# Kernel optimization log

Measured on AMD Instinct MI355X. Metric: run time of the kernel, lower is better.

The kernel has to match this reference:

```python
import jax, jax.numpy as jnp
import numpy as np

NUM_HEADS = 16

def setup_inputs() -> dict:
    key = jax.random.key(0)
    k1, k2, k3 = jax.random.split(key, 3)
    B, N, D = 2, 2048, 1024
    x = jax.random.normal(k1, (B, N, D), dtype=jnp.float32)
    w_qkv = jax.random.normal(k2, (D, 3 * D), dtype=jnp.float32) * (D ** -0.5)
    w_out = jax.random.normal(k3, (D, D), dtype=jnp.float32) * (D ** -0.5)
    return {"x": x, "w_qkv": w_qkv, "w_out": w_out}

def reference(x, w_qkv, w_out):
    B, N, D = x.shape
    H = NUM_HEADS
    d = D // H
    scale = d ** -0.5
    qkv = x @ w_qkv  # [B, N, 3D]
    q, k, v = jnp.split(qkv, 3, axis=-1)
    # b n (h d) -> b h n d
    split_heads = lambda t: t.reshape(B, N, H, d).transpose(0, 2, 1, 3)
    q, k, v = split_heads(q), split_heads(k), split_heads(v)
    dots = jnp.einsum('bhid,bhjd->bhij', q, k) * scale
    # causal mask: -inf above the diagonal
    causal = jnp.tril(jnp.ones((N, N), dtype=bool))
    dots = jnp.where(causal, dots, jnp.float32(-jnp.inf))
    attn = jax.nn.softmax(dots, axis=-1)
    out = jnp.einsum('bhij,bhjd->bhid', attn, v)
    out = out.transpose(0, 2, 1, 3).reshape(B, N, D)  # b h n d -> b n (h d)
    return out @ w_out
```

## Files before the change

### kernel.cpp

```cpp
#include <hip/hip_runtime.h>


typedef __bf16 bf16x8 __attribute__((ext_vector_type(8)));
typedef float f32x4 __attribute__((ext_vector_type(4)));
typedef unsigned int uint4v __attribute__((ext_vector_type(4)));

#define MFMA16(a, b, c) __builtin_amdgcn_mfma_f32_16x16x32_bf16((a), (b), (c), 0, 0, 0)

#define LDS_FENCE()                                   \
  do {                                                \
    asm volatile("s_waitcnt lgkmcnt(0)" ::: "memory");\
    __builtin_amdgcn_sched_barrier(0);                \
  } while (0)

__device__ __forceinline__ unsigned short f2bf(float f) {
  __bf16 h = (__bf16)f;
  return *(unsigned short*)&h;
}

__device__ __forceinline__ bf16x8 ones_frag() {
  uint4v u = {0x3F803F80u, 0x3F803F80u, 0x3F803F80u, 0x3F803F80u};
  return __builtin_bit_cast(bf16x8, u);
}

__global__ __launch_bounds__(256) void prep_kernel(
    const float* __restrict__ x, const float* __restrict__ wqkv,
    const float* __restrict__ wout, unsigned short* __restrict__ xb,
    unsigned short* __restrict__ wqkvT, unsigned short* __restrict__ woutT) {
  __shared__ float tile[32][33];
  const int id = blockIdx.x, t = threadIdx.x;
  if (id < 4096) {
    const int i = id * 256 + t;
    float4 v = ((const float4*)x)[i];
    ushort4 o;
    o.x = f2bf(v.x); o.y = f2bf(v.y); o.z = f2bf(v.z); o.w = f2bf(v.w);
    ((ushort4*)xb)[i] = o;
    return;
  }
  const int tx = t & 31, ty = t >> 5;
  const float* in; unsigned short* out;
  int C, scale_rows, bx, by;
  if (id < 7168) {
    const int q = id - 4096;
    in = wqkv; out = wqkvT; C = 3072; scale_rows = 1024;
    bx = q % 96; by = q / 96;
  } else {
    const int q = id - 7168;
    in = wout; out = woutT; C = 1024; scale_rows = 0;
    bx = q & 31; by = q >> 5;
  }
#pragma unroll
  for (int i = ty; i < 32; i += 8)
    tile[i][tx] = in[(size_t)(by * 32 + i) * C + bx * 32 + tx];
  __syncthreads();
#pragma unroll
  for (int i = ty; i < 32; i += 8) {
    const int orow = bx * 32 + i;
    const float s = (orow < scale_rows) ? 0.18033688f : 1.0f;
    out[(size_t)orow * 1024 + by * 32 + tx] = f2bf(tile[tx][i] * s);
  }
}

template <int MODE>
__global__ __launch_bounds__(256) void gemm128_kernel(
    const unsigned short* __restrict__ A,
    const unsigned short* __restrict__ BT,
    void* __restrict__ Cp, unsigned short* __restrict__ vTp,
    int M, int Nc, int K, int NX) {
  const int id0 = blockIdx.x;
  const int swz = (id0 & 7) * ((int)gridDim.x >> 3) + (id0 >> 3);
  const int bx = swz % NX, by = swz / NX;

  __shared__ unsigned short lA[128 * 64];
  __shared__ unsigned short lB[128 * 64];
  const int t = threadIdx.x;
  const int l = t & 63, g = l >> 4, c = l & 15;
  const int w = t >> 6;
  const int wm = (w >> 1) * 64, wn = (w & 1) * 64;
  const int bm = by * 128, bn = bx * 128;
  const int c7s = (c & 7);

  f32x4 acc[4][4] = {};

  for (int kk = 0; kk < K; kk += 64) {
    __syncthreads();
#pragma unroll
    for (int rd = 0; rd < 4; ++rd) {
      const int idx = rd * 256 + t;
      const int row = idx >> 3, ch = idx & 7;
      const int sc = (ch ^ (row & 7)) * 8;
      __builtin_amdgcn_global_load_lds(
          (const __attribute__((address_space(1))) void*)(
              A + (size_t)(bm + row) * K + kk + sc),
          (__attribute__((address_space(3))) void*)(lA + (idx & ~63) * 8),
          16, 0, 0);
      __builtin_amdgcn_global_load_lds(
          (const __attribute__((address_space(1))) void*)(
              BT + (size_t)(bn + row) * K + kk + sc),
          (__attribute__((address_space(3))) void*)(lB + (idx & ~63) * 8),
          16, 0, 0);
    }
    __syncthreads();

#pragma unroll
    for (int hh = 0; hh < 2; ++hh) {
      bf16x8 af[4], bfr[4];
#pragma unroll
      for (int mi = 0; mi < 4; ++mi)
        af[mi] = *(const bf16x8*)(lA + (wm + mi * 16 + c) * 64 +
                                  (((hh * 4 + g) ^ c7s) * 8));
#pragma unroll
      for (int ni = 0; ni < 4; ++ni)
        bfr[ni] = *(const bf16x8*)(lB + (wn + ni * 16 + c) * 64 +
                                   (((hh * 4 + g) ^ c7s) * 8));
#pragma unroll
      for (int mi = 0; mi < 4; ++mi)
#pragma unroll
        for (int ni = 0; ni < 4; ++ni)
          acc[mi][ni] = MFMA16(af[mi], bfr[ni], acc[mi][ni]);
    }
  }

  if (MODE == 0) {
    float* Cf = (float*)Cp;
#pragma unroll
    for (int mi = 0; mi < 4; ++mi)
#pragma unroll
      for (int r = 0; r < 4; ++r) {
        const int gr = bm + wm + mi * 16 + g * 4 + r;
#pragma unroll
        for (int ni = 0; ni < 4; ++ni)
          Cf[(size_t)gr * Nc + bn + wn + ni * 16 + c] = acc[mi][ni][r];
      }
  } else if (MODE == 2 && bn >= 2048) {
    const int bq = bm >> 11;
    const int nbase = bm - bq * 2048 + wm;
#pragma unroll
    for (int mi = 0; mi < 4; ++mi)
#pragma unroll
      for (int ni = 0; ni < 4; ++ni) {
        const int dimg = bn - 2048 + wn + ni * 16 + c;
        ushort4 pk;
        pk.x = f2bf(acc[mi][ni][0]); pk.y = f2bf(acc[mi][ni][1]);
        pk.z = f2bf(acc[mi][ni][2]); pk.w = f2bf(acc[mi][ni][3]);
        *(ushort4*)(vTp + ((size_t)(bq * 1024 + dimg)) * 2048 + nbase +
                    mi * 16 + g * 4) = pk;
      }
  } else {
    unsigned short* Cc = (unsigned short*)Cp;
#pragma unroll
    for (int mi = 0; mi < 4; ++mi)
#pragma unroll
      for (int r = 0; r < 4; ++r) {
        const int gr = bm + wm + mi * 16 + g * 4 + r;
#pragma unroll
        for (int ni = 0; ni < 4; ++ni)
          Cc[(size_t)gr * Nc + bn + wn + ni * 16 + c] = f2bf(acc[mi][ni][r]);
      }
  }
}

__global__ __launch_bounds__(256) void attn_kernel(
    const unsigned short* __restrict__ qkv,
    const unsigned short* __restrict__ vT,
    unsigned short* __restrict__ aout) {
  const int t = threadIdx.x, w = t >> 6, l = t & 63, g = l >> 4, c = l & 15;
  const int g4 = g * 4, c7 = c & 7;

  const int id0 = blockIdx.x;
  const int xcd = id0 & 7, pos = id0 >> 3;
  const int bh = xcd * 4 + (pos & 3);
  const int tile = 31 - (pos >> 2);
  const int b = bh >> 4, h = bh & 15;

  __shared__ __align__(16) unsigned short lK[2][64][64];
  __shared__ __align__(16) unsigned short lV[2][64][64];
  __shared__ __align__(16) unsigned short pl[4][16][72];

  const unsigned short* Qbase = qkv + (size_t)b * 2048 * 3072 + h * 64;
  const unsigned short* Kb = Qbase + 1024;
  const unsigned short* Vb = vT + ((size_t)b * 1024 + h * 64) * 2048;
  const bf16x8 vones = ones_frag();

#define KFRAG(row, half) (*(const bf16x8*)(Kb + (size_t)(row) * 3072 + (half) * 32 + g * 8))
#define VFRAG(dt, kvoff) (*(const bf16x8*)(Vb + (size_t)((dt) * 16 + c) * 2048 + (kvoff) + g * 8))

#define STAGE(dK, dV, kb_)                                                    \
  do {                                                                        \
    _Pragma("unroll")                                                         \
    for (int q = 0; q < 2; ++q) {                                             \
      const int idx = q * 256 + t;                                            \
      const int row = idx >> 3, ch = idx & 7;                                 \
      const int sc = (ch ^ (row & 7)) * 8;                                    \
      __builtin_amdgcn_global_load_lds(                                       \
          (const __attribute__((address_space(1))) void*)(                    \
              Kb + (size_t)(kb_ + row) * 3072 + sc),                          \
          (__attribute__((address_space(3))) void*)(                          \
              &(dK)[0][0] + (idx & ~63) * 8), 16, 0, 0);                      \
      __builtin_amdgcn_global_load_lds(                                       \
          (const __attribute__((address_space(1))) void*)(                    \
              Vb + (size_t)row * 2048 + (kb_) + sc),                          \
          (__attribute__((address_space(3))) void*)(                          \
              &(dV)[0][0] + (idx & ~63) * 8), 16, 0, 0);                      \
    }                                                                         \
  } while (0)

  const int q0 = tile * 64 + w * 16;
  const int qc = q0 + c;

  const bf16x8 bq0 = *(const bf16x8*)(Qbase + (size_t)qc * 3072 + g * 8);
  const bf16x8 bq1 = *(const bf16x8*)(Qbase + (size_t)qc * 3072 + 32 + g * 8);

  f32x4 o[4] = {};
  f32x4 dsum = {};

  if (tile > 0) {
    STAGE(lK[0], lV[0], 0);
    int cur = 0;
#pragma unroll 1
    for (int jb = 0; jb < tile; ++jb) {
      __syncthreads();
      if (jb + 1 < tile) STAGE(lK[cur ^ 1], lV[cur ^ 1], (jb + 1) * 64);

      const unsigned short* lk = &lK[cur][0][0];
      const unsigned short* lv = &lV[cur][0][0];

      bf16x8 ka[8];
#pragma unroll
      for (int n = 0; n < 4; ++n) {
        ka[2 * n]     = *(const bf16x8*)(lk + (16 * n + c) * 64 + ((g ^ c7) * 8));
        ka[2 * n + 1] = *(const bf16x8*)(lk + (16 * n + c) * 64 + (((4 + g) ^ c7) * 8));
      }
      bf16x8 bv[2][4];
#pragma unroll
      for (int ks = 0; ks < 2; ++ks)
#pragma unroll
        for (int dt = 0; dt < 4; ++dt)
          bv[ks][dt] = *(const bf16x8*)(lv + (dt * 16 + c) * 64 + (((ks * 4 + g) ^ c7) * 8));

      f32x4 s[4] = {};
#pragma unroll
      for (int n = 0; n < 4; ++n) {
        s[n] = MFMA16(ka[2 * n], bq0, s[n]);
        s[n] = MFMA16(ka[2 * n + 1], bq1, s[n]);
      }

#pragma unroll
      for (int n = 0; n < 4; ++n)
#pragma unroll
        for (int r = 0; r < 4; ++r)
          s[n][r] = exp2f(s[n][r]);

      LDS_FENCE();
#pragma unroll
      for (int n = 0; n < 4; ++n) {
        ushort4 pw;
        pw.x = f2bf(s[n][0]); pw.y = f2bf(s[n][1]);
        pw.z = f2bf(s[n][2]); pw.w = f2bf(s[n][3]);
        *(ushort4*)&pl[w][c][n * 16 + g4] = pw;
      }
      LDS_FENCE();
      const bf16x8 pa0 = *(const bf16x8*)&pl[w][c][g * 8];
      const bf16x8 pa1 = *(const bf16x8*)&pl[w][c][32 + g * 8];

      dsum = MFMA16(pa0, vones, dsum);
      dsum = MFMA16(pa1, vones, dsum);
#pragma unroll
      for (int dt = 0; dt < 4; ++dt) {
        o[dt] = MFMA16(pa0, bv[0][dt], o[dt]);
        o[dt] = MFMA16(pa1, bv[1][dt], o[dt]);
      }
      cur ^= 1;
    }
  }

  const int ndiag = 1 + (w >> 1);
#pragma unroll 1
  for (int j = 0; j < ndiag; ++j) {
    const int kb = tile * 64 + j * 32;
    const bf16x8 k00 = KFRAG(kb + c, 0), k01 = KFRAG(kb + c, 1);
    const bf16x8 k10 = KFRAG(kb + 16 + c, 0), k11 = KFRAG(kb + 16 + c, 1);
    const bf16x8 bv0 = VFRAG(0, kb), bv1 = VFRAG(1, kb);
    const bf16x8 bv2 = VFRAG(2, kb), bv3 = VFRAG(3, kb);

    f32x4 s0 = {}, s1 = {};
    s0 = MFMA16(k00, bq0, s0);
    s0 = MFMA16(k01, bq1, s0);
    s1 = MFMA16(k10, bq0, s1);
    s1 = MFMA16(k11, bq1, s1);

    float p0[4], p1[4];
#pragma unroll
    for (int r = 0; r < 4; ++r) {
      p0[r] = (kb + g4 + r <= qc) ? exp2f(s0[r]) : 0.0f;
      p1[r] = (kb + 16 + g4 + r <= qc) ? exp2f(s1[r]) : 0.0f;
    }

    LDS_FENCE();
    ushort4 pw;
    pw.x = f2bf(p0[0]); pw.y = f2bf(p0[1]); pw.z = f2bf(p0[2]); pw.w = f2bf(p0[3]);
    *(ushort4*)&pl[w][c][g4] = pw;
    pw.x = f2bf(p1[0]); pw.y = f2bf(p1[1]); pw.z = f2bf(p1[2]); pw.w = f2bf(p1[3]);
    *(ushort4*)&pl[w][c][16 + g4] = pw;
    LDS_FENCE();
    const bf16x8 pa = *(const bf16x8*)&pl[w][c][g * 8];

    dsum = MFMA16(pa, vones, dsum);
    o[0] = MFMA16(pa, bv0, o[0]);
    o[1] = MFMA16(pa, bv1, o[1]);
    o[2] = MFMA16(pa, bv2, o[2]);
    o[3] = MFMA16(pa, bv3, o[3]);
  }

#pragma unroll
  for (int r = 0; r < 4; ++r) {
    const float invr = 1.0f / dsum[r];
    const size_t row = (size_t)(b * 2048 + q0 + g4 + r);
#pragma unroll
    for (int dt = 0; dt < 4; ++dt)
      aout[row * 1024 + h * 64 + dt * 16 + c] = f2bf(o[dt][r] * invr);
  }
#undef KFRAG
#undef VFRAG
#undef STAGE
}

extern "C" void kernel_launch(void* const* d_in, const int* in_sizes, int n_in,
                              void* d_out, int out_size, void* d_ws, size_t ws_size,
                              hipStream_t stream) {
  const float* x = (const float*)d_in[0];
  const float* wqkv = (const float*)d_in[1];
  const float* wout = (const float*)d_in[2];
  float* out = (float*)d_out;

  unsigned short* ws = (unsigned short*)d_ws;
  unsigned short* xb = ws;
  unsigned short* wqkvT = xb + (size_t)4096 * 1024;
  unsigned short* woutT = wqkvT + (size_t)3072 * 1024;
  unsigned short* qkv = woutT + (size_t)1024 * 1024;
  unsigned short* vT = qkv + (size_t)4096 * 3072;
  unsigned short* aout = vT + (size_t)2 * 1024 * 2048;

  prep_kernel<<<8192, 256, 0, stream>>>(x, wqkv, wout, xb, wqkvT, woutT);
  gemm128_kernel<2><<<768, 256, 0, stream>>>(xb, wqkvT, qkv, vT, 4096, 3072, 1024, 24);
  attn_kernel<<<1024, 256, 0, stream>>>(qkv, vT, aout);
  gemm128_kernel<0><<<256, 256, 0, stream>>>(aout, woutT, out, nullptr, 4096, 1024, 1024, 8);
}
```

Before: 108.5 us.

## Replace QKV GEMM with 256x256 tile, 8-wave, double-buffered direct-to-LDS pipeline

The QKV projection GEMM moves from a 128x128, 4-wave kernel to a dedicated 256x256, 8-wave kernel. Tiles are loaded with global_load_lds straight into swizzled, double-buffered LDS, and the MFMA quadrants are interleaved with the next tile's loads, using barriers and s_setprio to overlap memory and compute. The goal is more operand reuse per LDS byte and hidden global load latency. In exchange the grid shrinks to 192 blocks, which fills fewer CUs on a 256-CU part, and register pressure at 512 threads is high.

```diff
diff --git a/kernel.cpp b/kernel.cpp
--- a/kernel.cpp
+++ b/kernel.cpp
@@ -61,12 +61,175 @@
   }
 }
 
-template <int MODE>
+__global__ __launch_bounds__(512) void gemm256_kernel(
+    const unsigned short* __restrict__ A,
+    const unsigned short* __restrict__ BT,
+    unsigned short* __restrict__ Cc,
+    unsigned short* __restrict__ vTp) {
+  const int id0 = blockIdx.x;
+  const int swz = (id0 & 7) * 24 + (id0 >> 3);
+  const int bx = swz % 12, by = swz / 12;
+  const int bm = by * 256, bn = bx * 256;
+
+  __shared__ unsigned short sA[2][2][128 * 64];
+  __shared__ unsigned short sB[2][2][128 * 64];
+
+  const int t = threadIdx.x;
+  const int l = t & 63, g = l >> 4, c = l & 15, c7 = c & 7;
+  const int wid = t >> 6, wr = wid >> 2, wc = wid & 3;
+
+  f32x4 acc[8][4] = {};
+  bf16x8 af[4][2], bfr[4][2];
+
+#define STG(dst, Mat, rowb, kt)                                               \
+  do {                                                                        \
+    _Pragma("unroll")                                                         \
+    for (int qq = 0; qq < 2; ++qq) {                                          \
+      const int idx = qq * 512 + t;                                           \
+      const int row = idx >> 3;                                               \
+      const int sc = ((idx & 7) ^ (row & 7)) * 8;                             \
+      __builtin_amdgcn_global_load_lds(                                       \
+          (const __attribute__((address_space(1))) void*)(                    \
+              (Mat) + (size_t)((rowb) + row) * 1024 + (kt) * 64 + sc),        \
+          (__attribute__((address_space(3))) void*)((dst) + (idx & ~63) * 8), \
+          16, 0, 0);                                                          \
+    }                                                                         \
+  } while (0)
+
+#define LDAQ(buf, qd)                                                         \
+  do {                                                                        \
+    _Pragma("unroll")                                                         \
+    for (int mi = 0; mi < 4; ++mi) {                                          \
+      const unsigned short* p =                                               \
+          &sA[buf][wr][0] + ((qd) * 64 + mi * 16 + c) * 64;                   \
+      af[mi][0] = *(const bf16x8*)(p + (g ^ c7) * 8);                         \
+      af[mi][1] = *(const bf16x8*)(p + ((4 + g) ^ c7) * 8);                   \
+    }                                                                         \
+  } while (0)
+
+#define LDBQ(buf, qd)                                                         \
+  do {                                                                        \
+    _Pragma("unroll")                                                         \
+    for (int nj = 0; nj < 2; ++nj) {                                          \
+      const unsigned short* p =                                               \
+          &sB[buf][wc >> 1][0] +                                              \
+          ((wc & 1) * 64 + ((qd) * 2 + nj) * 16 + c) * 64;                    \
+      bfr[(qd) * 2 + nj][0] = *(const bf16x8*)(p + (g ^ c7) * 8);             \
+      bfr[(qd) * 2 + nj][1] = *(const bf16x8*)(p + ((4 + g) ^ c7) * 8);       \
+    }                                                                         \
+  } while (0)
+
+#define MFMAQ(qm, qn)                                                         \
+  do {                                                                        \
+    _Pragma("unroll")                                                         \
+    for (int mi = 0; mi < 4; ++mi) {                                          \
+      _Pragma("unroll")                                                       \
+      for (int nj = 0; nj < 2; ++nj) {                                        \
+        f32x4 a0 = acc[(qm) * 4 + mi][(qn) * 2 + nj];                         \
+        a0 = MFMA16(af[mi][0], bfr[(qn) * 2 + nj][0], a0);                    \
+        a0 = MFMA16(af[mi][1], bfr[(qn) * 2 + nj][1], a0);                    \
+        acc[(qm) * 4 + mi][(qn) * 2 + nj] = a0;                               \
+      }                                                                       \
+    }                                                                         \
+  } while (0)
+
+#define BAR_OPEN()                                          \
+  do {                                                      \
+    __builtin_amdgcn_sched_barrier(0);                      \
+    __builtin_amdgcn_s_barrier();                           \
+    asm volatile("s_waitcnt lgkmcnt(0)" ::: "memory");      \
+    __builtin_amdgcn_sched_barrier(0);                      \
+    __builtin_amdgcn_s_setprio(1);                          \
+  } while (0)
+
+#define BAR_CLOSE()                                         \
+  do {                                                      \
+    __builtin_amdgcn_s_setprio(0);                          \
+    __builtin_amdgcn_sched_barrier(0);                      \
+    __builtin_amdgcn_s_barrier();                           \
+  } while (0)
+
+#define VMW4() asm volatile("s_waitcnt vmcnt(4)" ::: "memory")
+
+  STG(&sB[0][0][0], BT, bn, 0);
+  STG(&sB[0][1][0], BT, bn + 128, 0);
+  STG(&sA[0][0][0], A, bm, 0);
+  STG(&sA[0][1][0], A, bm + 128, 0);
+  STG(&sB[1][0][0], BT, bn, 1);
+  STG(&sB[1][1][0], BT, bn + 128, 1);
+  VMW4();
+  __builtin_amdgcn_s_barrier();
+
+#pragma unroll 1
+  for (int it = 0; it < 8; ++it) {
+    const int kt1 = 2 * it + 1;
+    const int kt2 = (2 * it + 2 < 15) ? 2 * it + 2 : 15;
+    const int kt3 = (2 * it + 3 < 15) ? 2 * it + 3 : 15;
+    LDAQ(0, 0); LDBQ(0, 0);
+    STG(&sA[1][0][0], A, bm, kt1);
+    BAR_OPEN(); MFMAQ(0, 0); BAR_CLOSE();
+    LDBQ(0, 1);
+    STG(&sA[1][1][0], A, bm + 128, kt1);
+    BAR_OPEN(); MFMAQ(0, 1); BAR_CLOSE();
+    LDAQ(0, 1);
+    STG(&sB[0][0][0], BT, bn, kt2);
+    BAR_OPEN(); MFMAQ(1, 0); BAR_CLOSE();
+    STG(&sB[0][1][0], BT, bn + 128, kt2);
+    VMW4();
+    BAR_OPEN(); MFMAQ(1, 1); BAR_CLOSE();
+    LDAQ(1, 0); LDBQ(1, 0);
+    STG(&sA[0][0][0], A, bm, kt2);
+    BAR_OPEN(); MFMAQ(0, 0); BAR_CLOSE();
+    LDBQ(1, 1);
+    STG(&sA[0][1][0], A, bm + 128, kt2);
+    BAR_OPEN(); MFMAQ(0, 1); BAR_CLOSE();
+    LDAQ(1, 1);
+    STG(&sB[1][0][0], BT, bn, kt3);
+    BAR_OPEN(); MFMAQ(1, 0); BAR_CLOSE();
+    STG(&sB[1][1][0], BT, bn + 128, kt3);
+    VMW4();
+    BAR_OPEN(); MFMAQ(1, 1); BAR_CLOSE();
+  }
+
+  if (bn >= 2048) {
+    const int bq = bm >> 11;
+    const int nb = (bm & 2047) + wr * 128;
+#pragma unroll
+    for (int mi8 = 0; mi8 < 8; ++mi8)
+#pragma unroll
+      for (int ni = 0; ni < 4; ++ni) {
+        const int dimg = bn - 2048 + wc * 64 + ni * 16 + c;
+        ushort4 pk;
+        pk.x = f2bf(acc[mi8][ni][0]); pk.y = f2bf(acc[mi8][ni][1]);
+        pk.z = f2bf(acc[mi8][ni][2]); pk.w = f2bf(acc[mi8][ni][3]);
+        *(ushort4*)(vTp + ((size_t)(bq * 1024 + dimg)) * 2048 + nb +
+                    mi8 * 16 + g * 4) = pk;
+      }
+  } else {
+#pragma unroll
+    for (int mi8 = 0; mi8 < 8; ++mi8)
+#pragma unroll
+      for (int r = 0; r < 4; ++r) {
+        const int gr = bm + wr * 128 + mi8 * 16 + g * 4 + r;
+#pragma unroll
+        for (int ni = 0; ni < 4; ++ni)
+          Cc[(size_t)gr * 3072 + bn + wc * 64 + ni * 16 + c] =
+              f2bf(acc[mi8][ni][r]);
+      }
+  }
+#undef STG
+#undef LDAQ
+#undef LDBQ
+#undef MFMAQ
+#undef BAR_OPEN
+#undef BAR_CLOSE
+#undef VMW4
+}
+
 __global__ __launch_bounds__(256) void gemm128_kernel(
     const unsigned short* __restrict__ A,
     const unsigned short* __restrict__ BT,
-    void* __restrict__ Cp, unsigned short* __restrict__ vTp,
-    int M, int Nc, int K, int NX) {
+    float* __restrict__ Cf, int M, int Nc, int K, int NX) {
   const int id0 = blockIdx.x;
   const int swz = (id0 & 7) * ((int)gridDim.x >> 3) + (id0 >> 3);
   const int bx = swz % NX, by = swz / NX;
@@ -121,43 +284,15 @@
     }
   }
 
-  if (MODE == 0) {
-    float* Cf = (float*)Cp;
-#pragma unroll
-    for (int mi = 0; mi < 4; ++mi)
-#pragma unroll
-      for (int r = 0; r < 4; ++r) {
-        const int gr = bm + wm + mi * 16 + g * 4 + r;
-#pragma unroll
-        for (int ni = 0; ni < 4; ++ni)
-          Cf[(size_t)gr * Nc + bn + wn + ni * 16 + c] = acc[mi][ni][r];
-      }
-  } else if (MODE == 2 && bn >= 2048) {
-    const int bq = bm >> 11;
-    const int nbase = bm - bq * 2048 + wm;
-#pragma unroll
-    for (int mi = 0; mi < 4; ++mi)
-#pragma unroll
-      for (int ni = 0; ni < 4; ++ni) {
-        const int dimg = bn - 2048 + wn + ni * 16 + c;
-        ushort4 pk;
-        pk.x = f2bf(acc[mi][ni][0]); pk.y = f2bf(acc[mi][ni][1]);
-        pk.z = f2bf(acc[mi][ni][2]); pk.w = f2bf(acc[mi][ni][3]);
-        *(ushort4*)(vTp + ((size_t)(bq * 1024 + dimg)) * 2048 + nbase +
-                    mi * 16 + g * 4) = pk;
-      }
-  } else {
-    unsigned short* Cc = (unsigned short*)Cp;
-#pragma unroll
-    for (int mi = 0; mi < 4; ++mi)
-#pragma unroll
-      for (int r = 0; r < 4; ++r) {
-        const int gr = bm + wm + mi * 16 + g * 4 + r;
-#pragma unroll
-        for (int ni = 0; ni < 4; ++ni)
-          Cc[(size_t)gr * Nc + bn + wn + ni * 16 + c] = f2bf(acc[mi][ni][r]);
-      }
-  }
+#pragma unroll
+  for (int mi = 0; mi < 4; ++mi)
+#pragma unroll
+    for (int r = 0; r < 4; ++r) {
+      const int gr = bm + wm + mi * 16 + g * 4 + r;
+#pragma unroll
+      for (int ni = 0; ni < 4; ++ni)
+        Cf[(size_t)gr * Nc + bn + wn + ni * 16 + c] = acc[mi][ni][r];
+    }
 }
 
 __global__ __launch_bounds__(256) void attn_kernel(
@@ -342,7 +477,7 @@
   unsigned short* aout = vT + (size_t)2 * 1024 * 2048;
 
   prep_kernel<<<8192, 256, 0, stream>>>(x, wqkv, wout, xb, wqkvT, woutT);
-  gemm128_kernel<2><<<768, 256, 0, stream>>>(xb, wqkvT, qkv, vT, 4096, 3072, 1024, 24);
+  gemm256_kernel<<<192, 512, 0, stream>>>(xb, wqkvT, qkv, vT);
   attn_kernel<<<1024, 256, 0, stream>>>(qkv, vT, aout);
-  gemm128_kernel<0><<<256, 256, 0, stream>>>(aout, woutT, out, nullptr, 4096, 1024, 1024, 8);
-}
+  gemm128_kernel<<<256, 256, 0, stream>>>(aout, woutT, out, 4096, 1024, 1024, 8);
+}
```

Measured after the change: 118.3 us. +9.1%, slower.
